# Kernel optimization log

Hardware: AMD Instinct MI355X
Metric: run time of the kernel (lower is better)

## Reference

```python
import jax, jax.numpy as jnp
import numpy as np

STRIDE = 16
SIZES = np.array([128.0, 256.0, 512.0], np.float32)
RATIOS = np.array([0.5, 1.0, 2.0], np.float32)
N_POS, N_NEG = 32, 32          # n_sample=64, pos_ratio=0.5
POS_THR, NEG_THR = 0.7, 0.2
W_CONF, W_REG = 1.0, 5.0


def _conv(x, w, b, stride, pad):
    y = jax.lax.conv_general_dilated(x, w, (stride, stride), [(pad, pad), (pad, pad)],
                                     dimension_numbers=('NCHW', 'OIHW', 'NCHW'))
    return y + b[None, :, None, None]


def _anchors(fw, fh, stride):
    # 9 anchors per center: 3 sizes x 3 aspect ratios
    ws = (SIZES[:, None] * np.sqrt(RATIOS)[None, :]).reshape(-1)
    hs = (SIZES[:, None] / np.sqrt(RATIOS)[None, :]).reshape(-1)
    wh = jnp.asarray(np.stack([ws, hs], -1))                      # (9,2)
    cx = (jnp.arange(fw, dtype=jnp.float32) + 0.5) * stride
    cy = (jnp.arange(fh, dtype=jnp.float32) + 0.5) * stride
    gx, gy = jnp.meshgrid(cx, cy, indexing='ij')                  # x-major, like the torch list comp
    ctr = jnp.stack([gx, gy], -1)[:, :, None, :]                  # (fw,fh,1,2)
    tl = ctr - wh / 2.0
    xywh = jnp.concatenate([tl, jnp.broadcast_to(wh, tl.shape)], -1)  # (fw,fh,9,4)
    return xywh.reshape(-1, 4)


def _xywh_to_xyxy(b):
    return jnp.concatenate([b[:, :2], b[:, :2] + b[:, 2:]], -1)


def _iou(a, b):  # a [N,4], b [M,4], xyxy
    lt = jnp.maximum(a[:, None, :2], b[None, :, :2])
    rb = jnp.minimum(a[:, None, 2:], b[None, :, 2:])
    inter = jnp.clip(rb - lt, 0.0).prod(-1)
    aa = (a[:, 2] - a[:, 0]) * (a[:, 3] - a[:, 1])
    ab = (b[:, 2] - b[:, 0]) * (b[:, 3] - b[:, 1])
    return inter / (aa[:, None] + ab[None, :] - inter)


def _head_flat(y, per):  # [1, 9*per, H, W] -> [W*H*9, per], matching anchor flatten order
    _, _, H, W = y.shape
    return y[0].reshape(9, per, H, W).transpose(3, 2, 0, 1).reshape(-1, per)


def _apply_offsets(boxes, off):  # decode proposals from xyxy boxes + (dx,dy,dw,dh)
    w = boxes[:, 2] - boxes[:, 0]; h = boxes[:, 3] - boxes[:, 1]
    cx = boxes[:, 0] + 0.5 * w;    cy = boxes[:, 1] + 0.5 * h
    ncx = cx + off[:, 0] * w;      ncy = cy + off[:, 1] * h
    nw = w * jnp.exp(off[:, 2]);   nh = h * jnp.exp(off[:, 3])
    return jnp.stack([ncx - nw / 2, ncy - nh / 2, ncx + nw / 2, ncy + nh / 2], -1)


def _box_offset(anc, gt):
    aw = anc[:, 2] - anc[:, 0]; ah = anc[:, 3] - anc[:, 1]
    acx = anc[:, 0] + 0.5 * aw; acy = anc[:, 1] + 0.5 * ah
    gw = gt[:, 2] - gt[:, 0];   gh = gt[:, 3] - gt[:, 1]
    gcx = gt[:, 0] + 0.5 * gw;  gcy = gt[:, 1] + 0.5 * gh
    return jnp.stack([(gcx - acx) / aw, (gcy - acy) / ah,
                      jnp.log(gw / aw), jnp.log(gh / ah)], -1)


def setup_inputs():
    key = jax.random.key(0)
    ks = jax.random.split(key, 12)
    img_data = jax.random.normal(ks[0], (1, 3, 1600, 1600), jnp.float32)
    x1 = jax.random.uniform(ks[1], (64,), minval=0.0, maxval=1400.0)
    y1 = jax.random.uniform(ks[2], (64,), minval=0.0, maxval=1400.0)
    bw = jax.random.uniform(ks[3], (64,), minval=32.0, maxval=200.0)
    bh = jax.random.uniform(ks[4], (64,), minval=32.0, maxval=200.0)
    gt_boxes = jnp.stack([x1, y1, x1 + bw, y1 + bh], -1)[None]   # [1,64,4], all valid (no -1 pad)
    gt_classes = jax.random.randint(ks[5], (1, 64), 1, 21, jnp.int32)
    def w(k, shape, fan):
        return jax.random.normal(k, shape, jnp.float32) * np.float32(np.sqrt(2.0 / fan))
    return dict(
        img_data=img_data, gt_boxes=gt_boxes, gt_classes=gt_classes,
        w1=w(ks[6], (64, 3, 7, 7), 3 * 49),      b1=jnp.zeros(64, jnp.float32),
        w2=w(ks[7], (256, 64, 3, 3), 64 * 9),    b2=jnp.zeros(256, jnp.float32),
        w_rpn=w(ks[8], (256, 256, 3, 3), 256 * 9), b_rpn=jnp.zeros(256, jnp.float32),
        w_cls=w(ks[9], (18, 256, 1, 1), 256),    b_cls=jnp.zeros(18, jnp.float32),
        w_reg=w(ks[10], (36, 256, 1, 1), 256),   b_reg=jnp.zeros(36, jnp.float32),
    )


def reference(img_data, gt_boxes, gt_classes, w1, b1, w2, b2, w_rpn, b_rpn, w_cls, b_cls, w_reg, b_reg):
    # --- feature extractor (total stride 16) ---
    fm = jax.nn.relu(_conv(img_data, w1, b1, 4, 3))
    fm = jax.nn.relu(_conv(fm, w2, b2, 4, 1))            # [1,256,100,100]
    H, W = fm.shape[2], fm.shape[3]
    # --- anchors + IoU matching ---
    anchors_xywh = _anchors(W, H, STRIDE)                # [N,4] xywh
    anchors_xyxy = _xywh_to_xyxy(anchors_xywh)
    gt = gt_boxes[0]                                     # [M,4], all valid
    ious = _iou(anchors_xyxy, gt)                        # [N,M]
    N = ious.shape[0]
    gt_max = ious.max(0)                                 # best iou per gt
    is_gt_best = (ious == gt_max[None, :]).any(1)        # torch: where(iou == gt_max)[0]
    anc_argmax = ious.argmax(1)
    anc_max = ious.max(1)
    labels = jnp.full((N,), -1.0, jnp.float32)
    labels = jnp.where(anc_max < NEG_THR, 0.0, labels)
    labels = jnp.where(is_gt_best, 1.0, labels)
    labels = jnp.where(anc_max > POS_THR, 1.0, labels)
    # --- deterministic pos/neg sampling (fixed sizes; replaces randperm subsampling) ---
    idx = jnp.arange(N, dtype=jnp.float32)
    _, pos_index = jax.lax.top_k(jnp.where(labels == 1.0, anc_max, -1.0), N_POS)
    _, neg_index = jax.lax.top_k(jnp.where(labels == 0.0, 1e6 - idx, -1e9), N_NEG)
    bboxes_pos = anchors_xyxy[pos_index]                 # box_convert(xywh->xyxy) of pos anchors
    # --- proposal module (RPN head) ---
    h = jax.nn.relu(_conv(fm, w_rpn, b_rpn, 1, 1))
    cls = _head_flat(_conv(h, w_cls, b_cls, 1, 0), 2)    # [N,2]
    reg = _head_flat(_conv(h, w_reg, b_reg, 1, 0), 4)    # [N,4]
    pos_score = cls[pos_index]
    neg_score = cls[neg_index]
    offset_pos = reg[pos_index]
    proposals = _apply_offsets(bboxes_pos, offset_pos)
    # --- losses ---
    gt_offset = _box_offset(bboxes_pos, gt[anc_argmax[pos_index]])
    logits = jnp.concatenate([pos_score, neg_score], 0)  # [64,2]
    tgt = jnp.concatenate([jnp.ones(N_POS, jnp.int32), jnp.zeros(N_NEG, jnp.int32)])
    logp = jax.nn.log_softmax(logits, -1)
    cls_loss = -logp[jnp.arange(N_POS + N_NEG), tgt].mean()
    d = gt_offset - offset_pos
    ad = jnp.abs(d)
    reg_loss = jnp.where(ad < 1.0, 0.5 * d * d, ad - 0.5).mean()
    total_rpn_loss = W_CONF * cls_loss + W_REG * reg_loss
    gt_cls_pos = gt_classes[0][anc_argmax[pos_index]]
    return (total_rpn_loss, fm, proposals, pos_index, gt_cls_pos)
```

## Files before the change

### kernel.cpp

```cpp
#include <hip/hip_runtime.h>
#include <math.h>


#define CAP 4096

typedef __attribute__((ext_vector_type(8))) short bf16x8;
typedef __attribute__((ext_vector_type(4))) float f32x4;

#define OFF_F1T     0
#define OFF_HBUF    0
#define OFF_FMT     5171328
#define OFF_CPART   6503040
#define OFF_RPART   7223040
#define OFF_WA1     8663040
#define OFF_W9_2    8672448
#define OFF_W9_3    8746176
#define OFF_WTC     9041088
#define OFF_WTG     9045696
#define OFF_AARG    9054912
#define OFF_NEGM    9144912
#define OFF_POSM    9147728
#define OFF_GTMAX   9150544
#define OFF_CANDS   9150688
#define OFF_CANDI   9154784

__device__ __forceinline__ unsigned short f2bf(float f) {
    unsigned int u = __float_as_uint(f);
    u += 0x7fffu + ((u >> 16) & 1u);
    return (unsigned short)(u >> 16);
}

__device__ __forceinline__ void anchor_box(int i, float& x0, float& y0,
                                           float& x1, float& y1, float& area) {
#pragma clang fp contract(off)
    const float sizes[3]  = {128.f, 256.f, 512.f};
    const float ratios[3] = {0.5f, 1.f, 2.f};
    int a = i % 9;
    int q = i / 9;
    int iy = q % 100;
    int ix = q / 100;
    int s = a / 3, r = a % 3;
    float sq = sqrtf(ratios[r]);
    float w = sizes[s] * sq;
    float h = sizes[s] / sq;
    float cx = ((float)ix + 0.5f) * 16.0f;
    float cy = ((float)iy + 0.5f) * 16.0f;
    x0 = cx - w * 0.5f;
    y0 = cy - h * 0.5f;
    x1 = x0 + w;
    y1 = y0 + h;
    area = (x1 - x0) * (y1 - y0);
}

__device__ __forceinline__ float iou_one(float ax0, float ay0, float ax1, float ay1, float aa,
                                         float bx0, float by0, float bx1, float by1, float ab) {
#pragma clang fp contract(off)
    float ltx = fmaxf(ax0, bx0), lty = fmaxf(ay0, by0);
    float rbx = fminf(ax1, bx1), rby = fminf(ay1, by1);
    float iw = fmaxf(rbx - ltx, 0.0f);
    float ih = fmaxf(rby - lty, 0.0f);
    float inter = iw * ih;
    return inter / ((aa + ab) - inter);
}

__global__ __launch_bounds__(256) void setup_kernel(const float* __restrict__ wc, float* __restrict__ wtc,
                                                    const float* __restrict__ wg, float* __restrict__ wtg,
                                                    const float* __restrict__ w1, unsigned short* __restrict__ wa1,
                                                    const float* __restrict__ w2, unsigned short* __restrict__ w9_2,
                                                    const float* __restrict__ wr, unsigned short* __restrict__ w9_3,
                                                    unsigned int* __restrict__ f1t_u, unsigned int* __restrict__ fmt_u,
                                                    unsigned int* __restrict__ gtmax) {
    int i = blockIdx.x * 256 + threadIdx.x;
    if (i < 65) { gtmax[i] = 0u; return; }
    i -= 65;
    if (i < 103040) {
        if (i < 51328) {
            int p = i >> 5, part = i & 31;
            int x, y;
            if (p < 804) { y = (p < 402) ? 0 : 401; x = p % 402; }
            else { int j = p - 804; x = (j < 400) ? 0 : 401; y = 1 + (j % 400); }
            f1t_u[(y * 402 + x) * 32 + part] = 0u;
        } else {
            int i2 = i - 51328;
            int p = i2 >> 7, part = i2 & 127;
            int x, y;
            if (p < 204) { y = (p < 102) ? 0 : 101; x = p % 102; }
            else { int j = p - 204; x = (j < 100) ? 0 : 101; y = 1 + (j % 100); }
            fmt_u[(y * 102 + x) * 128 + part] = 0u;
        }
        return;
    }
    i -= 103040;
    if (i < 4608) { int c = i / 256, k = i - c * 256; wtc[k * 18 + c] = wc[i]; return; }
    i -= 4608;
    if (i < 9216) { int c = i / 256, k = i - c * 256; wtg[k * 36 + c] = wg[i]; return; }
    i -= 9216;
    if (i < 12288) {
        int oc = i / 192, k = i - oc * 192;
        int q = k >> 3, kx = k & 7;
        int ky = q / 3, ic = q - (q / 3) * 3;
        wa1[i] = (q < 21 && kx < 7) ? f2bf(w1[oc * 147 + ic * 49 + ky * 7 + kx])
                                    : (unsigned short)0;
        return;
    }
    i -= 12288;
    if (i < 147456) {
        int kk = i / 16384; int rem = i - kk * 16384;
        int oc = rem / 64, ic = rem - oc * 64;
        w9_2[i] = f2bf(w2[(oc * 64 + ic) * 9 + kk]);
        return;
    }
    i -= 147456;
    if (i < 589824) {
        int cc = i / 16384; int rem = i - cc * 16384;
        int oc = rem / 64, icl = rem - oc * 64;
        int kk = cc / 4, ch = cc - kk * 4;
        w9_3[i] = f2bf(wr[(oc * 256 + ch * 64 + icl) * 9 + kk]);
    }
}

__global__ __launch_bounds__(256) void conv1_mfma(const float* __restrict__ img,
                                                  const unsigned short* __restrict__ wA,
                                                  const float* __restrict__ bias,
                                                  unsigned short* __restrict__ f1t) {
    __shared__ unsigned short win[24 * 260];
    __shared__ unsigned short tileT[64 * 72];
    int t = threadIdx.x;
    int wave = t >> 6, lane = t & 63;
    int quad = lane >> 4, l16 = lane & 15;
    int oy = blockIdx.y;
    int ox0 = blockIdx.x * 64;
    int gx0 = ox0 * 4 - 3;
    int gy0 = 4 * oy - 3;

    for (int r = 0; r < 24; r++) {
        int ky = r / 3, ic = r - (r / 3) * 3;
        int gy = gy0 + ky;
        bool rowok = (r < 21) && (gy >= 0) && (gy < 1600);
        {
            int gx = gx0 + t;
            float v = (rowok && gx >= 0 && gx < 1600) ? img[(ic * 1600 + gy) * 1600 + gx] : 0.f;
            win[r * 260 + t] = f2bf(v);
        }
        if (t < 4) {
            int c2 = 256 + t;
            int gx = gx0 + c2;
            float v = (rowok && gx >= 0 && gx < 1600) ? img[(ic * 1600 + gy) * 1600 + gx] : 0.f;
            win[r * 260 + c2] = f2bf(v);
        }
    }
    bf16x8 afr[6];
    {
        const bf16x8* ap = (const bf16x8*)(wA + (wave * 16 + l16) * 192 + quad * 8);
#pragma unroll
        for (int c = 0; c < 6; c++) afr[c] = ap[c * 4];
    }
    __syncthreads();

    f32x4 acc[4];
#pragma unroll
    for (int j = 0; j < 4; j++) acc[j] = (f32x4){0.f, 0.f, 0.f, 0.f};
#pragma unroll
    for (int ch = 0; ch < 6; ch++) {
        const unsigned short* wrow = win + (ch * 4 + quad) * 260;
#pragma unroll
        for (int j = 0; j < 4; j++) {
            int px = j * 16 + l16;
            const unsigned long long* bp = (const unsigned long long*)(wrow + 4 * px);
            union { unsigned long long u[2]; bf16x8 v; } uu;
            uu.u[0] = bp[0];
            uu.u[1] = bp[1];
            acc[j] = __builtin_amdgcn_mfma_f32_16x16x32_bf16(afr[ch], uu.v, acc[j], 0, 0, 0);
        }
    }
#pragma unroll
    for (int reg = 0; reg < 4; reg++) {
        int oc = wave * 16 + quad * 4 + reg;
        float bv = bias[oc];
#pragma unroll
        for (int j = 0; j < 4; j++) {
            int px = j * 16 + l16;
            tileT[px * 72 + oc] = f2bf(fmaxf(acc[j][reg] + bv, 0.f));
        }
    }
    __syncthreads();
    int px = t >> 2, part = t & 3;
    int ox = ox0 + px;
    if (ox < 400) {
        int row = (oy + 1) * 402 + ox + 1;
        uint4 v0 = *(const uint4*)(tileT + px * 72 + part * 16);
        uint4 v1 = *(const uint4*)(tileT + px * 72 + part * 16 + 8);
        *(uint4*)(f1t + row * 64 + part * 16) = v0;
        *(uint4*)(f1t + row * 64 + part * 16 + 8) = v1;
    }
}

template<int ICC, int RS, int S, bool WRT>
__global__ __launch_bounds__(256, 2) void conv_gemm(const unsigned short* __restrict__ Bt,
                                                    const unsigned short* __restrict__ A9,
                                                    const float* __restrict__ bias,
                                                    float* __restrict__ outF,
                                                    unsigned short* __restrict__ outT) {
    const int NC = ICC / 64;
    const int HC = S * 24 + 3;
    const int LROW = ICC + 8;
    __shared__ unsigned short blds[3 * HC * LROW];
    __shared__ unsigned short alds[256 * 72];
    int t = threadIdx.x;
    int xs = blockIdx.x, y = blockIdx.y;

    const int CHW = ICC / 8;
    for (int idx = t; idx < 3 * HC * CHW; idx += 256) {
        int row = idx / CHW, e = idx - row * CHW;
        int ky = row / HC, c = row - ky * HC;
        const uint4* src = (const uint4*)(Bt + ((size_t)(S * y + ky) * RS + S * xs * 25 + c) * ICC) + e;
        *(uint4*)(blds + row * LROW + e * 8) = *src;
    }
    int wave = t >> 6, lane = t & 63;
    int quad = lane >> 4, l16 = lane & 15;
    int oc0 = wave * 64;
    int pxe0 = min(l16, 24);
    int pxe1 = min(16 + l16, 24);

    f32x4 acc[4][2];
#pragma unroll
    for (int mt = 0; mt < 4; mt++)
#pragma unroll
        for (int j = 0; j < 2; j++) acc[mt][j] = (f32x4){0.f, 0.f, 0.f, 0.f};

    const unsigned short* a0 = alds + (oc0 + l16) * 72 + quad * 8;
    for (int cc = 0; cc < 9 * NC; cc++) {
        int pass = cc / NC, ch = cc - pass * NC;
        int ky = pass / 3, kx = pass - (pass / 3) * 3;
        __syncthreads();
        const uint4* asrc = (const uint4*)(A9 + (size_t)cc * 16384);
#pragma unroll
        for (int i = 0; i < 8; i++) {
            int e = i * 256 + t;
            *(uint4*)(alds + (e >> 3) * 72 + (e & 7) * 8) = asrc[e];
        }
        __syncthreads();
        const unsigned short* b0 = blds + (ky * HC + S * pxe0 + kx) * LROW + ch * 64 + quad * 8;
        const unsigned short* b1 = blds + (ky * HC + S * pxe1 + kx) * LROW + ch * 64 + quad * 8;
#pragma unroll
        for (int kcl = 0; kcl < 2; kcl++) {
            bf16x8 bf0 = *(const bf16x8*)(b0 + kcl * 32);
            bf16x8 bf1 = *(const bf16x8*)(b1 + kcl * 32);
#pragma unroll
            for (int mt = 0; mt < 4; mt++) {
                bf16x8 af = *(const bf16x8*)(a0 + mt * 16 * 72 + kcl * 32);
                acc[mt][0] = __builtin_amdgcn_mfma_f32_16x16x32_bf16(af, bf0, acc[mt][0], 0, 0, 0);
                acc[mt][1] = __builtin_amdgcn_mfma_f32_16x16x32_bf16(af, bf1, acc[mt][1], 0, 0, 0);
            }
        }
    }
#pragma unroll
    for (int mt = 0; mt < 4; mt++) {
#pragma unroll
        for (int reg = 0; reg < 4; reg++) {
            int oc = oc0 + mt * 16 + quad * 4 + reg;
            float bv = bias[oc];
#pragma unroll
            for (int j = 0; j < 2; j++) {
                int pl = j * 16 + l16;
                if (pl < 25) {
                    int p = y * 100 + xs * 25 + pl;
                    float v = fmaxf(acc[mt][j][reg] + bv, 0.f);
                    outF[oc * 10000 + p] = v;
                    if (WRT) {
                        int r = (y + 1) * 102 + xs * 25 + pl + 1;
                        outT[r * 256 + oc] = f2bf(v);
                    }
                }
            }
        }
    }
}

__global__ __launch_bounds__(64) void head_kernel(const float* __restrict__ hbuf,
                                                  const float* __restrict__ wtc,
                                                  const float* __restrict__ wtg,
                                                  float* __restrict__ cpart,
                                                  float* __restrict__ rpart) {
    int p = blockIdx.x * 64 + threadIdx.x;
    int ch = blockIdx.y;
    int ic0 = ch * 64;
    if (p >= 10000) return;
    float acc[54];
#pragma unroll
    for (int j = 0; j < 54; j++) acc[j] = 0.f;
    for (int ic = 0; ic < 64; ic++) {
        float v = hbuf[(ic0 + ic) * 10000 + p];
        const float* wc_ = wtc + (ic0 + ic) * 18;
#pragma unroll
        for (int j = 0; j < 18; j++) acc[j] += v * wc_[j];
        const float* wg_ = wtg + (ic0 + ic) * 36;
#pragma unroll
        for (int j = 0; j < 36; j++) acc[18 + j] += v * wg_[j];
    }
    for (int j = 0; j < 18; j++) cpart[(ch * 18 + j) * 10000 + p] = acc[j];
    for (int j = 0; j < 36; j++) rpart[(ch * 36 + j) * 10000 + p] = acc[18 + j];
}

__global__ __launch_bounds__(256) void iou_pass1(const float* __restrict__ gt,
                                                 int* __restrict__ aarg,
                                                 unsigned int* __restrict__ gtmax) {
    __shared__ float sg[64][4];
    __shared__ float sarea[64];
    __shared__ unsigned int smax[64];
    int t = threadIdx.x;
    if (t < 64) {
#pragma clang fp contract(off)
        float b0 = gt[t * 4 + 0], b1 = gt[t * 4 + 1];
        float b2 = gt[t * 4 + 2], b3 = gt[t * 4 + 3];
        sg[t][0] = b0; sg[t][1] = b1; sg[t][2] = b2; sg[t][3] = b3;
        sarea[t] = (b2 - b0) * (b3 - b1);
        smax[t] = 0u;
    }
    __syncthreads();
    int i = blockIdx.x * 256 + t;
    int iq = min(i, 89999);
    float x0, y0, x1, y1, aa;
    anchor_box(iq, x0, y0, x1, y1, aa);
    float best = -1.f;
    int bestj = 0;
    for (int j = 0; j < 64; j++) {
        float v = iou_one(x0, y0, x1, y1, aa, sg[j][0], sg[j][1], sg[j][2], sg[j][3], sarea[j]);
        if (v > best) { best = v; bestj = j; }
        float vm = v;
#pragma unroll
        for (int off = 32; off > 0; off >>= 1) vm = fmaxf(vm, __shfl_xor(vm, off));
        if ((t & 63) == 0) atomicMax(&smax[j], __float_as_uint(vm));
    }
    if (i < 90000) aarg[i] = bestj;
    __syncthreads();
    if (t < 64) atomicMax(&gtmax[t], smax[t]);
}

__global__ __launch_bounds__(256) void iou_pass2(const float* __restrict__ gt,
                                                 const unsigned int* __restrict__ gtmax,
                                                 unsigned long long* __restrict__ negmask,
                                                 unsigned long long* __restrict__ posmask,
                                                 float* __restrict__ cand_s,
                                                 int* __restrict__ cand_i,
                                                 unsigned int* __restrict__ cnt) {
    __shared__ float sg[64][4];
    __shared__ float sarea[64];
    __shared__ float sgm[64];
    int t = threadIdx.x;
    if (t < 64) {
#pragma clang fp contract(off)
        float b0 = gt[t * 4 + 0], b1 = gt[t * 4 + 1];
        float b2 = gt[t * 4 + 2], b3 = gt[t * 4 + 3];
        sg[t][0] = b0; sg[t][1] = b1; sg[t][2] = b2; sg[t][3] = b3;
        sarea[t] = (b2 - b0) * (b3 - b1);
        sgm[t] = __uint_as_float(gtmax[t]);
    }
    __syncthreads();
    int i = blockIdx.x * 256 + t;
    if (i >= 90000) return;
    float x0, y0, x1, y1, aa;
    anchor_box(i, x0, y0, x1, y1, aa);
    float best = -1.f;
    bool isbest = false;
    for (int j = 0; j < 64; j++) {
        float v = iou_one(x0, y0, x1, y1, aa, sg[j][0], sg[j][1], sg[j][2], sg[j][3], sarea[j]);
        if (v > best) best = v;
        if (v == sgm[j]) isbest = true;
    }
    float label = -1.f;
    if (best < 0.2f) label = 0.f;
    if (isbest) label = 1.f;
    if (best > 0.7f) label = 1.f;
    unsigned long long negb = __ballot(label == 0.f);
    unsigned long long posb = __ballot(label == 1.f);
    if ((t & 63) == 0) { negmask[i >> 6] = negb; posmask[i >> 6] = posb; }
    if (label == 1.f) {
        unsigned int p = atomicAdd(cnt, 1u);
        if (p < CAP) { cand_s[p] = best; cand_i[p] = i; }
    }
}

__device__ __forceinline__ unsigned long long shflx64(unsigned long long v, int m) {
    int lo = __shfl_xor((int)(unsigned)(v & 0xFFFFFFFFull), m);
    int hi = __shfl_xor((int)(unsigned)(v >> 32), m);
    return ((unsigned long long)(unsigned)hi << 32) | (unsigned)lo;
}

__device__ int wave_first32(const unsigned long long* __restrict__ mask,
                            bool invert, int* __restrict__ outIdx, int lane) {
    const int NW = 1407;
    const int WPT = 22;
    unsigned long long mw[WPT];
    int cnt = 0;
#pragma unroll
    for (int u = 0; u < WPT; u++) {
        int w = lane * WPT + u;
        unsigned long long m = 0ull;
        if (w < NW) {
            m = mask[w];
            if (invert) m = ~m;
            if (w == NW - 1) m &= 0xFFFFull;
        }
        mw[u] = m;
        cnt += __builtin_popcountll(m);
    }
    int inc = cnt;
#pragma unroll
    for (int off = 1; off < 64; off <<= 1) {
        int v = __shfl_up(inc, off);
        if (lane >= off) inc += v;
    }
    int total = __shfl(inc, 63);
    int pref = inc - cnt;
    if (pref < 32) {
#pragma unroll
        for (int u = 0; u < WPT; u++) {
            unsigned long long m = mw[u];
            int wbase = (lane * WPT + u) * 64;
            while (m && pref < 32) {
                int b = __builtin_ctzll(m);
                outIdx[pref++] = wbase + b;
                m &= m - 1;
            }
        }
    }
    return total;
}

__global__ __launch_bounds__(64) void tail_kernel(const unsigned long long* __restrict__ negmask,
                                                  const unsigned long long* __restrict__ posmask,
                                                  const float* __restrict__ cand_s,
                                                  const int* __restrict__ cand_i,
                                                  const unsigned int* __restrict__ cnt,
                                                  const float* __restrict__ cpart,
                                                  const float* __restrict__ rpart,
                                                  const float* __restrict__ bcls,
                                                  const float* __restrict__ breg,
                                                  const int* __restrict__ aarg,
                                                  const float* __restrict__ gt,
                                                  const int* __restrict__ gtc,
                                                  float* __restrict__ out) {
    __shared__ unsigned long long keys[CAP + 32];
    __shared__ int sfill[32];
    __shared__ int spidx[32];
    __shared__ int snidx[32];
    int lane = threadIdx.x;

    int ncand = min((int)*cnt, CAP);
    for (int c = lane; c < ncand; c += 64) {
        unsigned u = __float_as_uint(cand_s[c]);
        u ^= (u & 0x80000000u) ? 0xFFFFFFFFu : 0x80000000u;
        keys[c] = ((unsigned long long)u << 32) | (0xFFFFFFFFu - (unsigned)cand_i[c]);
    }
    int ntot = ncand;
    if (ncand < 32) {
        int tot = wave_first32(posmask, true, sfill, lane);
        int nfill = min(tot, 32);
        unsigned um1 = __float_as_uint(-1.0f) ^ 0xFFFFFFFFu;
        for (int k2 = lane; k2 < nfill; k2 += 64)
            keys[ncand + k2] = ((unsigned long long)um1 << 32) | (0xFFFFFFFFu - (unsigned)sfill[k2]);
        ntot += nfill;
    }

    unsigned long long lk = 0ull; int ls = -1;
    for (int c = lane; c < ntot; c += 64) {
        unsigned long long k = keys[c];
        if (k > lk) { lk = k; ls = c; }
    }
    for (int s = 0; s < 32; s++) {
        unsigned long long mk = lk;
#pragma unroll
        for (int off = 1; off < 64; off <<= 1) {
            unsigned long long o = shflx64(mk, off);
            if (o > mk) mk = o;
        }
        if (lk == mk && mk != 0ull) {
            spidx[s] = (int)(0xFFFFFFFFu - (unsigned)(mk & 0xFFFFFFFFull));
            keys[ls] = 0ull;
            lk = 0ull; ls = -1;
            for (int c = lane; c < ntot; c += 64) {
                unsigned long long k = keys[c];
                if (k > lk) { lk = k; ls = c; }
            }
        }
    }

    int totn = wave_first32(negmask, false, snidx, lane);
    if (lane == 0) {
        int nf = min(totn, 32);
        for (int s = nf; s < 32; s++) snidx[s] = s;
    }

    {
#pragma clang fp contract(off)
        const int PROP_OFF = 1 + 2560000;
        int t = lane;
        int n = (t < 32) ? spidx[t] : snidx[t - 32];
        int a = n % 9;
        int q = n / 9;
        int iy = q % 100;
        int ix = q / 100;
        int p = iy * 100 + ix;

        float l0 = bcls[a * 2 + 0], l1 = bcls[a * 2 + 1];
        for (int c = 0; c < 4; c++) {
            l0 += cpart[(c * 18 + a * 2 + 0) * 10000 + p];
            l1 += cpart[(c * 18 + a * 2 + 1) * 10000 + p];
        }
        float m = fmaxf(l0, l1);
        float lse = m + logf(expf(l0 - m) + expf(l1 - m));
        float logp = ((t < 32) ? l1 : l0) - lse;
        float cls_sum = logp;
#pragma unroll
        for (int off = 32; off > 0; off >>= 1) cls_sum += __shfl_down(cls_sum, off);

        float reg_sum = 0.f;
        if (t < 32) {
            float offv[4];
#pragma unroll
            for (int k = 0; k < 4; k++) {
                float v = breg[a * 4 + k];
                for (int c = 0; c < 4; c++) v += rpart[(c * 36 + a * 4 + k) * 10000 + p];
                offv[k] = v;
            }
            float x0, y0, x1, y1, aa;
            anchor_box(n, x0, y0, x1, y1, aa);
            float w = x1 - x0, h = y1 - y0;
            float cx = x0 + 0.5f * w, cy = y0 + 0.5f * h;
            float ncx = cx + offv[0] * w, ncy = cy + offv[1] * h;
            float nw = w * expf(offv[2]), nh = h * expf(offv[3]);
            out[PROP_OFF + t * 4 + 0] = ncx - nw * 0.5f;
            out[PROP_OFF + t * 4 + 1] = ncy - nh * 0.5f;
            out[PROP_OFF + t * 4 + 2] = ncx + nw * 0.5f;
            out[PROP_OFF + t * 4 + 3] = ncy + nh * 0.5f;

            int j = aarg[n];
            float g0 = gt[j * 4 + 0], g1 = gt[j * 4 + 1];
            float g2 = gt[j * 4 + 2], g3 = gt[j * 4 + 3];
            float gw = g2 - g0, gh = g3 - g1;
            float gcx = g0 + 0.5f * gw, gcy = g1 + 0.5f * gh;
            float tg[4];
            tg[0] = (gcx - cx) / w;
            tg[1] = (gcy - cy) / h;
            tg[2] = logf(gw / w);
            tg[3] = logf(gh / h);
#pragma unroll
            for (int k = 0; k < 4; k++) {
                float d = tg[k] - offv[k];
                float ad = fabsf(d);
                reg_sum += (ad < 1.f) ? 0.5f * d * d : ad - 0.5f;
            }
            out[PROP_OFF + 128 + t] = (float)n;
            out[PROP_OFF + 160 + t] = (float)gtc[j];
        }
#pragma unroll
        for (int off = 32; off > 0; off >>= 1) reg_sum += __shfl_down(reg_sum, off);
        if (t == 0) {
            float cls_loss = -(cls_sum / 64.f);
            float reg_loss = reg_sum / 128.f;
            out[0] = cls_loss + 5.f * reg_loss;
        }
    }
}

extern "C" void kernel_launch(void* const* d_in, const int* in_sizes, int n_in,
                              void* d_out, int out_size, void* d_ws, size_t ws_size,
                              hipStream_t stream) {
    const float* img = (const float*)d_in[0];
    const float* gt  = (const float*)d_in[1];
    const int*   gtc = (const int*)d_in[2];
    const float* w1  = (const float*)d_in[3];
    const float* b1  = (const float*)d_in[4];
    const float* w2  = (const float*)d_in[5];
    const float* b2  = (const float*)d_in[6];
    const float* wr  = (const float*)d_in[7];
    const float* br  = (const float*)d_in[8];
    const float* wc  = (const float*)d_in[9];
    const float* bc  = (const float*)d_in[10];
    const float* wg  = (const float*)d_in[11];
    const float* bg  = (const float*)d_in[12];
    float* out = (float*)d_out;
    float* ws = (float*)d_ws;

    unsigned short* f1t  = (unsigned short*)(ws + OFF_F1T);
    unsigned short* fmt  = (unsigned short*)(ws + OFF_FMT);
    unsigned short* wa1  = (unsigned short*)(ws + OFF_WA1);
    unsigned short* w9_2 = (unsigned short*)(ws + OFF_W9_2);
    unsigned short* w9_3 = (unsigned short*)(ws + OFF_W9_3);
    float* hbuf  = ws + OFF_HBUF;
    float* cpart = ws + OFF_CPART;
    float* rpart = ws + OFF_RPART;
    float* wtc   = ws + OFF_WTC;
    float* wtg   = ws + OFF_WTG;
    int*   aarg  = (int*)(ws + OFF_AARG);
    unsigned long long* negm = (unsigned long long*)(ws + OFF_NEGM);
    unsigned long long* posm = (unsigned long long*)(ws + OFF_POSM);
    unsigned int* gtmax = (unsigned int*)(ws + OFF_GTMAX);
    unsigned int* cnt   = gtmax + 64;
    float* cands = ws + OFF_CANDS;
    int*   candi = (int*)(ws + OFF_CANDI);
    float* fm    = out + 1;

    setup_kernel<<<dim3(3385), dim3(256), 0, stream>>>(wc, wtc, wg, wtg, w1, wa1,
                                                       w2, w9_2, wr, w9_3,
                                                       (unsigned int*)f1t, (unsigned int*)fmt, gtmax);

    conv1_mfma<<<dim3(7, 400), dim3(256), 0, stream>>>(img, wa1, b1, f1t);
    conv_gemm<64, 402, 4, true><<<dim3(4, 100), dim3(256), 0, stream>>>(f1t, w9_2, b2, fm, fmt);
    conv_gemm<256, 102, 1, false><<<dim3(4, 100), dim3(256), 0, stream>>>(fmt, w9_3, br, hbuf, nullptr);
    head_kernel<<<dim3(157, 4), dim3(64), 0, stream>>>(hbuf, wtc, wtg, cpart, rpart);

    iou_pass1<<<dim3(352), dim3(256), 0, stream>>>(gt, aarg, gtmax);
    iou_pass2<<<dim3(352), dim3(256), 0, stream>>>(gt, gtmax, negm, posm, cands, candi, cnt);
    tail_kernel<<<dim3(1), dim3(64), 0, stream>>>(negm, posm, cands, candi, cnt,
                                                  cpart, rpart, bc, bg, aarg, gt, gtc, out);
}
```

Before: 290.5 us.

## Load conv weights in MFMA fragment order directly from global, swizzle LDS, batch loads

Reorders the packed conv2/conv3 weight layout into MFMA fragment order so each wave reads its A operands straight from global memory. This drops the per-chunk LDS staging of A and the two barriers per chunk. It also XOR-swizzles the stride-4 B tile in LDS to cut bank conflicts, and raises occupancy to 3 blocks per CU now that the A buffer in LDS is gone. Image loads in conv1 are batched into registers before the LDS writes, and the head kernel preloads 8 input values at a time to add memory-level parallelism. The cost is more register pressure and repeated global or L2 reads of the weights by every block.

```diff
diff --git a/kernel.cpp b/kernel.cpp
--- a/kernel.cpp
+++ b/kernel.cpp
@@ -105,17 +105,31 @@
     }
     i -= 12288;
     if (i < 147456) {
-        int kk = i / 16384; int rem = i - kk * 16384;
-        int oc = rem / 64, ic = rem - oc * 64;
-        w9_2[i] = f2bf(w2[(oc * 64 + ic) * 9 + kk]);
+        int cc = i >> 14;
+        int rem = i & 16383;
+        int ocT = rem >> 10;
+        int rem2 = rem & 1023;
+        int kcl = rem2 >> 9;
+        int lane = (rem2 & 511) >> 3;
+        int e = rem2 & 7;
+        int oc = ocT * 16 + (lane & 15);
+        int ic = kcl * 32 + (lane >> 4) * 8 + e;
+        w9_2[i] = f2bf(w2[(oc * 64 + ic) * 9 + cc]);
         return;
     }
     i -= 147456;
     if (i < 589824) {
-        int cc = i / 16384; int rem = i - cc * 16384;
-        int oc = rem / 64, icl = rem - oc * 64;
-        int kk = cc / 4, ch = cc - kk * 4;
-        w9_3[i] = f2bf(wr[(oc * 256 + ch * 64 + icl) * 9 + kk]);
+        int cc = i >> 14;
+        int rem = i & 16383;
+        int ocT = rem >> 10;
+        int rem2 = rem & 1023;
+        int kcl = rem2 >> 9;
+        int lane = (rem2 & 511) >> 3;
+        int e = rem2 & 7;
+        int kk = cc >> 2, chv = cc & 3;
+        int oc = ocT * 16 + (lane & 15);
+        int icl = kcl * 32 + (lane >> 4) * 8 + e;
+        w9_3[i] = f2bf(wr[(oc * 256 + chv * 64 + icl) * 9 + kk]);
     }
 }
 
@@ -133,21 +147,23 @@
     int gx0 = ox0 * 4 - 3;
     int gy0 = 4 * oy - 3;
 
-    for (int r = 0; r < 24; r++) {
+    int gx = gx0 + t;
+    bool xok = (gx >= 0) && (gx < 1600);
+    float v[21];
+#pragma unroll
+    for (int r = 0; r < 21; r++) {
         int ky = r / 3, ic = r - (r / 3) * 3;
         int gy = gy0 + ky;
-        bool rowok = (r < 21) && (gy >= 0) && (gy < 1600);
-        {
-            int gx = gx0 + t;
-            float v = (rowok && gx >= 0 && gx < 1600) ? img[(ic * 1600 + gy) * 1600 + gx] : 0.f;
-            win[r * 260 + t] = f2bf(v);
-        }
-        if (t < 4) {
-            int c2 = 256 + t;
-            int gx = gx0 + c2;
-            float v = (rowok && gx >= 0 && gx < 1600) ? img[(ic * 1600 + gy) * 1600 + gx] : 0.f;
-            win[r * 260 + c2] = f2bf(v);
-        }
+        v[r] = (xok && gy >= 0 && gy < 1600) ? img[(ic * 1600 + gy) * 1600 + gx] : 0.f;
+    }
+    float vt = 0.f;
+    int rt = t >> 2, ctl = 256 + (t & 3);
+    if (rt < 21) {
+        int ky = rt / 3, ic = rt - (rt / 3) * 3;
+        int gy = gy0 + ky;
+        int gxt = gx0 + ctl;
+        vt = (gxt >= 0 && gxt < 1600 && gy >= 0 && gy < 1600)
+                 ? img[(ic * 1600 + gy) * 1600 + gxt] : 0.f;
     }
     bf16x8 afr[6];
     {
@@ -155,6 +171,13 @@
 #pragma unroll
         for (int c = 0; c < 6; c++) afr[c] = ap[c * 4];
     }
+#pragma unroll
+    for (int r = 0; r < 21; r++) win[r * 260 + t] = f2bf(v[r]);
+    if (rt < 21) win[rt * 260 + ctl] = f2bf(vt);
+    win[5460 + t] = 0;
+    win[5460 + 256 + t] = 0;
+    win[5460 + 512 + t] = 0;
+    if (t < 12) win[5460 + 768 + t] = 0;
     __syncthreads();
 
     f32x4 acc[4];
@@ -196,7 +219,7 @@
 }
 
 template<int ICC, int RS, int S, bool WRT>
-__global__ __launch_bounds__(256, 2) void conv_gemm(const unsigned short* __restrict__ Bt,
+__global__ __launch_bounds__(256, 3) void conv_gemm(const unsigned short* __restrict__ Bt,
                                                     const unsigned short* __restrict__ A9,
                                                     const float* __restrict__ bias,
                                                     float* __restrict__ outF,
@@ -204,23 +227,40 @@
     const int NC = ICC / 64;
     const int HC = S * 24 + 3;
     const int LROW = ICC + 8;
+    const int CHW = ICC / 8;
+    const int TOT = 3 * HC * CHW;
+    const int NIT = (TOT + 255) / 256;
     __shared__ unsigned short blds[3 * HC * LROW];
-    __shared__ unsigned short alds[256 * 72];
     int t = threadIdx.x;
     int xs = blockIdx.x, y = blockIdx.y;
 
-    const int CHW = ICC / 8;
-    for (int idx = t; idx < 3 * HC * CHW; idx += 256) {
-        int row = idx / CHW, e = idx - row * CHW;
-        int ky = row / HC, c = row - ky * HC;
-        const uint4* src = (const uint4*)(Bt + ((size_t)(S * y + ky) * RS + S * xs * 25 + c) * ICC) + e;
-        *(uint4*)(blds + row * LROW + e * 8) = *src;
-    }
+    uint4 stg[NIT];
+#pragma unroll
+    for (int i = 0; i < NIT; i++) {
+        int idx = t + i * 256;
+        if (idx < TOT) {
+            int row = idx / CHW, e = idx - row * CHW;
+            int ky = row / HC, c = row - ky * HC;
+            stg[i] = ((const uint4*)(Bt + ((size_t)(S * y + ky) * RS + S * xs * 25 + c) * ICC))[e];
+        }
+    }
+#pragma unroll
+    for (int i = 0; i < NIT; i++) {
+        int idx = t + i * 256;
+        if (idx < TOT) {
+            int row = idx / CHW, e = idx - row * CHW;
+            int ky = row / HC, c = row - ky * HC;
+            int e2 = (S == 4) ? (e ^ ((c >> 2) & 7)) : e;
+            *(uint4*)(blds + row * LROW + e2 * 8) = stg[i];
+        }
+    }
+
     int wave = t >> 6, lane = t & 63;
     int quad = lane >> 4, l16 = lane & 15;
     int oc0 = wave * 64;
     int pxe0 = min(l16, 24);
     int pxe1 = min(16 + l16, 24);
+    int sw0 = pxe0 & 7, sw1 = pxe1 & 7;
 
     f32x4 acc[4][2];
 #pragma unroll
@@ -228,29 +268,30 @@
 #pragma unroll
         for (int j = 0; j < 2; j++) acc[mt][j] = (f32x4){0.f, 0.f, 0.f, 0.f};
 
-    const unsigned short* a0 = alds + (oc0 + l16) * 72 + quad * 8;
+    const bf16x8* Av = (const bf16x8*)A9;
+    int abase = wave * 512 + lane;
+    __syncthreads();
+
     for (int cc = 0; cc < 9 * NC; cc++) {
         int pass = cc / NC, ch = cc - pass * NC;
         int ky = pass / 3, kx = pass - (pass / 3) * 3;
-        __syncthreads();
-        const uint4* asrc = (const uint4*)(A9 + (size_t)cc * 16384);
-#pragma unroll
-        for (int i = 0; i < 8; i++) {
-            int e = i * 256 + t;
-            *(uint4*)(alds + (e >> 3) * 72 + (e & 7) * 8) = asrc[e];
-        }
-        __syncthreads();
-        const unsigned short* b0 = blds + (ky * HC + S * pxe0 + kx) * LROW + ch * 64 + quad * 8;
-        const unsigned short* b1 = blds + (ky * HC + S * pxe1 + kx) * LROW + ch * 64 + quad * 8;
+        bf16x8 af[4][2];
+#pragma unroll
+        for (int mt = 0; mt < 4; mt++)
+#pragma unroll
+            for (int kcl = 0; kcl < 2; kcl++)
+                af[mt][kcl] = Av[abase + cc * 2048 + (mt * 2 + kcl) * 64];
+        int rb0 = (ky * HC + S * pxe0 + kx) * LROW + ch * 64;
+        int rb1 = (ky * HC + S * pxe1 + kx) * LROW + ch * 64;
 #pragma unroll
         for (int kcl = 0; kcl < 2; kcl++) {
-            bf16x8 bf0 = *(const bf16x8*)(b0 + kcl * 32);
-            bf16x8 bf1 = *(const bf16x8*)(b1 + kcl * 32);
+            int ck = kcl * 4 + quad;
+            bf16x8 bf0 = *(const bf16x8*)(blds + rb0 + ((S == 4) ? (ck ^ sw0) : ck) * 8);
+            bf16x8 bf1 = *(const bf16x8*)(blds + rb1 + ((S == 4) ? (ck ^ sw1) : ck) * 8);
 #pragma unroll
             for (int mt = 0; mt < 4; mt++) {
-                bf16x8 af = *(const bf16x8*)(a0 + mt * 16 * 72 + kcl * 32);
-                acc[mt][0] = __builtin_amdgcn_mfma_f32_16x16x32_bf16(af, bf0, acc[mt][0], 0, 0, 0);
-                acc[mt][1] = __builtin_amdgcn_mfma_f32_16x16x32_bf16(af, bf1, acc[mt][1], 0, 0, 0);
+                acc[mt][0] = __builtin_amdgcn_mfma_f32_16x16x32_bf16(af[mt][kcl], bf0, acc[mt][0], 0, 0, 0);
+                acc[mt][1] = __builtin_amdgcn_mfma_f32_16x16x32_bf16(af[mt][kcl], bf1, acc[mt][1], 0, 0, 0);
             }
         }
     }
@@ -289,14 +330,19 @@
     float acc[54];
 #pragma unroll
     for (int j = 0; j < 54; j++) acc[j] = 0.f;
-    for (int ic = 0; ic < 64; ic++) {
-        float v = hbuf[(ic0 + ic) * 10000 + p];
-        const float* wc_ = wtc + (ic0 + ic) * 18;
-#pragma unroll
-        for (int j = 0; j < 18; j++) acc[j] += v * wc_[j];
-        const float* wg_ = wtg + (ic0 + ic) * 36;
-#pragma unroll
-        for (int j = 0; j < 36; j++) acc[18 + j] += v * wg_[j];
+    for (int ic = 0; ic < 64; ic += 8) {
+        float vv[8];
+#pragma unroll
+        for (int u = 0; u < 8; u++) vv[u] = hbuf[(ic0 + ic + u) * 10000 + p];
+#pragma unroll
+        for (int u = 0; u < 8; u++) {
+            const float* wc_ = wtc + (ic0 + ic + u) * 18;
+#pragma unroll
+            for (int j = 0; j < 18; j++) acc[j] += vv[u] * wc_[j];
+            const float* wg_ = wtg + (ic0 + ic + u) * 36;
+#pragma unroll
+            for (int j = 0; j < 36; j++) acc[18 + j] += vv[u] * wg_[j];
+        }
     }
     for (int j = 0; j < 18; j++) cpart[(ch * 18 + j) * 10000 + p] = acc[j];
     for (int j = 0; j < 36; j++) rpart[(ch * 36 + j) * 10000 + p] = acc[18 + j];
```

After: 303.5 us. +4.5%, slower.
